# Kernel tuning notes

Measured on AMD Instinct MI355X. Metric: run time of the kernel, lower is better.

## Reference

```python
import jax, jax.numpy as jnp
import numpy as np


def setup_inputs() -> dict:
    key = jax.random.key(0)
    ks = jax.random.split(key, 8)
    N, T, U = 8, 200, 50
    E = D = J = 512
    V = 500
    s = lambda k, shape, fan_in: jax.random.normal(k, shape, jnp.float32) / np.sqrt(fan_in)
    return {
        "encoder_out": jax.random.normal(ks[0], (N, T, E), jnp.float32),
        "decoder_out": jax.random.normal(ks[1], (N, U, D), jnp.float32),
        "W_enc": s(ks[2], (J, E), E),
        "b_enc": jax.random.normal(ks[3], (J,), jnp.float32) * 0.01,
        "W_dec": s(ks[4], (J, D), D),
        "b_dec": jax.random.normal(ks[5], (J,), jnp.float32) * 0.01,
        "W_out": s(ks[6], (V, J), J),
        "b_out": jax.random.normal(ks[7], (V,), jnp.float32) * 0.01,
    }


def reference(encoder_out, decoder_out, W_enc, b_enc, W_dec, b_dec, W_out, b_out):
    # Project encoder (N,T,E)->(N,T,J) and decoder (N,U,D)->(N,U,J).
    enc_p = jnp.einsum("nte,je->ntj", encoder_out, W_enc) + b_enc
    dec_p = jnp.einsum("nud,jd->nuj", decoder_out, W_dec) + b_dec
    # Broadcast add -> (N,T,U,J), tanh, then linear to vocab -> (N,T,U,V).
    activations = jnp.tanh(enc_p[:, :, None, :] + dec_p[:, None, :, :])
    logits = jnp.einsum("ntuj,vj->ntuv", activations, W_out) + b_out
    return logits
```

## Files before the change

kernel.cpp:

```cpp
#include <hip/hip_runtime.h>
#include <hip/hip_bf16.h>
#include <stdint.h>

#define JD 512
#define VV 500

typedef short short8 __attribute__((ext_vector_type(8)));
typedef short short4v __attribute__((ext_vector_type(4)));
typedef float floatx4 __attribute__((ext_vector_type(4)));

__device__ inline short f2bf(float f) {
    uint32_t u = __float_as_uint(f);
    uint32_t r = (u + 0x7FFFu + ((u >> 16) & 1u)) >> 16;
    return (short)r;
}

__device__ inline float fast_tanh(float x) {
    float e = __builtin_amdgcn_exp2f(x * 2.8853900817779268f);
    return 1.0f - 2.0f * __builtin_amdgcn_rcpf(e + 1.0f);
}

__global__ __launch_bounds__(256) void prep_kernel(
    const float* __restrict__ Wout, short* __restrict__ WbF)
{
    int j = blockIdx.x * 256 + threadIdx.x;
    int l16  = j & 15;
    int q4   = (j >> 4) & 3;
    int ks   = (j >> 6) & 15;
    int vblk = j >> 10;
    int v  = vblk * 16 + l16;
    int k0 = ks * 32 + q4 * 8;
    short8 o;
    if (v < VV) {
        const float4* p = (const float4*)(Wout + (size_t)v * JD + k0);
        float4 a = p[0], b = p[1];
        o[0] = f2bf(a.x); o[1] = f2bf(a.y); o[2] = f2bf(a.z); o[3] = f2bf(a.w);
        o[4] = f2bf(b.x); o[5] = f2bf(b.y); o[6] = f2bf(b.z); o[7] = f2bf(b.w);
    } else {
        o = (short8){0,0,0,0,0,0,0,0};
    }
    *(short8*)(WbF + (size_t)j * 8) = o;
}

#define PST 72
__global__ __launch_bounds__(256) void proj_gemm(
    const float* __restrict__ enc, const float* __restrict__ dec,
    const float* __restrict__ Wenc, const float* __restrict__ Wdec,
    const float* __restrict__ b_enc, const float* __restrict__ b_dec,
    float* __restrict__ enc_p, float* __restrict__ dec_p)
{
    __shared__ short As[64 * PST];
    __shared__ short Bs[64 * PST];
    int bx = blockIdx.x, by = blockIdx.y;
    const float* A; const float* W; const float* bias; float* C; int M;
    if (bx < 25) { A = enc; W = Wenc; bias = b_enc; C = enc_p; M = 1600; }
    else { bx -= 25; A = dec; W = Wdec; bias = b_dec; C = dec_p; M = 400; }

    int tid = threadIdx.x;
    int lane = tid & 63, wv = tid >> 6;
    int wm = wv >> 1, wn = wv & 1;
    int l16 = lane & 15, q4 = lane >> 4;

    int ra = tid >> 2, ha = tid & 3;
    int m_st = bx * 64 + ra;
    bool valid = m_st < M;
    int wrow = by * 64 + ra;

    floatx4 acc[2][2];
    #pragma unroll
    for (int a = 0; a < 2; a++)
        #pragma unroll
        for (int b = 0; b < 2; b++) acc[a][b] = (floatx4){0.f, 0.f, 0.f, 0.f};

    for (int kk = 0; kk < 8; kk++) {
        int k0 = kk * 64;
        __syncthreads();
        {
            float4 v0 = make_float4(0.f, 0.f, 0.f, 0.f);
            float4 v1 = v0, v2 = v0, v3 = v0;
            if (valid) {
                const float4* p = (const float4*)(A + (size_t)m_st * JD + k0 + ha * 16);
                v0 = p[0]; v1 = p[1]; v2 = p[2]; v3 = p[3];
            }
            short8 o0, o1;
            o0[0] = f2bf(v0.x); o0[1] = f2bf(v0.y); o0[2] = f2bf(v0.z); o0[3] = f2bf(v0.w);
            o0[4] = f2bf(v1.x); o0[5] = f2bf(v1.y); o0[6] = f2bf(v1.z); o0[7] = f2bf(v1.w);
            o1[0] = f2bf(v2.x); o1[1] = f2bf(v2.y); o1[2] = f2bf(v2.z); o1[3] = f2bf(v2.w);
            o1[4] = f2bf(v3.x); o1[5] = f2bf(v3.y); o1[6] = f2bf(v3.z); o1[7] = f2bf(v3.w);
            *(short8*)&As[ra * PST + ha * 16]     = o0;
            *(short8*)&As[ra * PST + ha * 16 + 8] = o1;

            const float4* pb = (const float4*)(W + (size_t)wrow * JD + k0 + ha * 16);
            float4 w0 = pb[0], w1 = pb[1], w2 = pb[2], w3 = pb[3];
            short8 p0, p1;
            p0[0] = f2bf(w0.x); p0[1] = f2bf(w0.y); p0[2] = f2bf(w0.z); p0[3] = f2bf(w0.w);
            p0[4] = f2bf(w1.x); p0[5] = f2bf(w1.y); p0[6] = f2bf(w1.z); p0[7] = f2bf(w1.w);
            p1[0] = f2bf(w2.x); p1[1] = f2bf(w2.y); p1[2] = f2bf(w2.z); p1[3] = f2bf(w2.w);
            p1[4] = f2bf(w3.x); p1[5] = f2bf(w3.y); p1[6] = f2bf(w3.z); p1[7] = f2bf(w3.w);
            *(short8*)&Bs[ra * PST + ha * 16]     = p0;
            *(short8*)&Bs[ra * PST + ha * 16 + 8] = p1;
        }
        __syncthreads();
        #pragma unroll
        for (int h2 = 0; h2 < 2; h2++) {
            short8 af[2], bf[2];
            #pragma unroll
            for (int im = 0; im < 2; im++)
                af[im] = *(const short8*)&As[(wm * 32 + im * 16 + l16) * PST + h2 * 32 + q4 * 8];
            #pragma unroll
            for (int in = 0; in < 2; in++)
                bf[in] = *(const short8*)&Bs[(wn * 32 + in * 16 + l16) * PST + h2 * 32 + q4 * 8];
            #pragma unroll
            for (int im = 0; im < 2; im++)
                #pragma unroll
                for (int in = 0; in < 2; in++)
                    acc[im][in] = __builtin_amdgcn_mfma_f32_16x16x32_bf16(
                        af[im], bf[in], acc[im][in], 0, 0, 0);
        }
    }
    #pragma unroll
    for (int im = 0; im < 2; im++) {
        int mb = bx * 64 + wm * 32 + im * 16 + q4 * 4;
        #pragma unroll
        for (int rr = 0; rr < 4; rr++) {
            int m = mb + rr;
            if (m < M) {
                #pragma unroll
                for (int in = 0; in < 2; in++) {
                    int j = by * 64 + wn * 32 + in * 16 + l16;
                    C[(size_t)m * JD + j] = acc[im][in][rr] + bias[j];
                }
            }
        }
    }
}

#define AST 520
__global__ __launch_bounds__(256, 2) void fused_joiner(
    const float* __restrict__ enc_p, const float* __restrict__ dec_p,
    const short* __restrict__ WbF, const float* __restrict__ b_out,
    float* __restrict__ out)
{
    __shared__ short As[64 * AST];
    int tid = threadIdx.x;
    int bx = blockIdx.x;

    {
        int rsub = tid >> 7;
        int jf = (tid & 127) * 4;
        #pragma unroll 4
        for (int pass = 0; pass < 32; pass++) {
            int row = pass * 2 + rsub;
            int m = bx * 64 + row;
            int er = m / 50;
            int n  = m / 10000;
            int dr = n * 50 + (m - er * 50);
            float4 e = *(const float4*)(enc_p + (size_t)er * JD + jf);
            float4 d = *(const float4*)(dec_p + (size_t)dr * JD + jf);
            short4v o;
            o[0] = f2bf(fast_tanh(e.x + d.x));
            o[1] = f2bf(fast_tanh(e.y + d.y));
            o[2] = f2bf(fast_tanh(e.z + d.z));
            o[3] = f2bf(fast_tanh(e.w + d.w));
            *(short4v*)&As[row * AST + jf] = o;
        }
    }
    __syncthreads();

    int lane = tid & 63, wn = tid >> 6;
    int l16 = lane & 15, q4 = lane >> 4;

    floatx4 acc[4][8];
    #pragma unroll
    for (int a = 0; a < 4; a++)
        #pragma unroll
        for (int b = 0; b < 8; b++) acc[a][b] = (floatx4){0.f, 0.f, 0.f, 0.f};

    int abase[4];
    #pragma unroll
    for (int im = 0; im < 4; im++)
        abase[im] = (im * 16 + l16) * AST + q4 * 8;
    int boff[8];
    #pragma unroll
    for (int in = 0; in < 8; in++)
        boff[in] = (wn * 8 + in) * 8192 + q4 * 128 + l16 * 8;

    short8 b0[8], b1[8];
    #pragma unroll
    for (int in = 0; in < 8; in++)
        b0[in] = *(const short8*)(WbF + boff[in]);

    for (int ks = 0; ks < 16; ks += 2) {
        #pragma unroll
        for (int in = 0; in < 8; in++)
            b1[in] = *(const short8*)(WbF + boff[in] + (ks + 1) * 512);
        {
            int k0 = ks * 32;
            short8 af[4];
            #pragma unroll
            for (int im = 0; im < 4; im++)
                af[im] = *(const short8*)&As[abase[im] + k0];
            #pragma unroll
            for (int im = 0; im < 4; im++)
                #pragma unroll
                for (int in = 0; in < 8; in++)
                    acc[im][in] = __builtin_amdgcn_mfma_f32_16x16x32_bf16(
                        af[im], b0[in], acc[im][in], 0, 0, 0);
        }
        if (ks + 2 < 16) {
            #pragma unroll
            for (int in = 0; in < 8; in++)
                b0[in] = *(const short8*)(WbF + boff[in] + (ks + 2) * 512);
        }
        {
            int k1 = (ks + 1) * 32;
            short8 af[4];
            #pragma unroll
            for (int im = 0; im < 4; im++)
                af[im] = *(const short8*)&As[abase[im] + k1];
            #pragma unroll
            for (int im = 0; im < 4; im++)
                #pragma unroll
                for (int in = 0; in < 8; in++)
                    acc[im][in] = __builtin_amdgcn_mfma_f32_16x16x32_bf16(
                        af[im], b1[in], acc[im][in], 0, 0, 0);
        }
    }

    float bo[8];
    #pragma unroll
    for (int in = 0; in < 8; in++) {
        int v = wn * 128 + in * 16 + l16;
        bo[in] = (v < VV) ? b_out[v] : 0.f;
    }
    #pragma unroll
    for (int im = 0; im < 4; im++) {
        int mb = bx * 64 + im * 16 + q4 * 4;
        #pragma unroll
        for (int rr = 0; rr < 4; rr++) {
            size_t orow = (size_t)(mb + rr) * VV;
            #pragma unroll
            for (int in = 0; in < 8; in++) {
                int v = wn * 128 + in * 16 + l16;
                if (v < VV) out[orow + v] = acc[im][in][rr] + bo[in];
            }
        }
    }
}

extern "C" void kernel_launch(void* const* d_in, const int* in_sizes, int n_in,
                              void* d_out, int out_size, void* d_ws, size_t ws_size,
                              hipStream_t stream)
{
    const float* enc   = (const float*)d_in[0];
    const float* dec   = (const float*)d_in[1];
    const float* Wenc  = (const float*)d_in[2];
    const float* b_enc = (const float*)d_in[3];
    const float* Wdec  = (const float*)d_in[4];
    const float* b_dec = (const float*)d_in[5];
    const float* Wout  = (const float*)d_in[6];
    const float* b_out = (const float*)d_in[7];
    float* out = (float*)d_out;

    char* ws = (char*)d_ws;
    short* WbF   = (short*)(ws + 0);
    float* enc_p = (float*)(ws + 524288);
    float* dec_p = (float*)(ws + 3801088);

    prep_kernel<<<128, 256, 0, stream>>>(Wout, WbF);
    proj_gemm<<<dim3(32, 8), 256, 0, stream>>>(enc, dec, Wenc, Wdec,
                                               b_enc, b_dec, enc_p, dec_p);
    fused_joiner<<<1250, 256, 0, stream>>>(enc_p, dec_p, WbF, b_out, out);
}
```

Baseline: 250.5 us.

## Split joiner tile across 8 waves, re-layout packed W_out, use nontemporal stores

The fused joiner block grows from 4 to 8 waves, each computing a 32x128 sub-tile instead of 64x128, so accumulators halve and more waves can be resident per CU. The packed bf16 W_out layout is reordered so each k-step's fragments for a wave are contiguous. The software double-buffering of B fragments is dropped. Output logits are written with nontemporal stores to avoid polluting cache. The cost is that each B fragment is now loaded by two waves instead of one, and latency hiding relies on occupancy rather than explicit prefetch.

```diff
diff --git a/kernel.cpp b/kernel.cpp
--- a/kernel.cpp
+++ b/kernel.cpp
@@ -24,11 +24,12 @@
     const float* __restrict__ Wout, short* __restrict__ WbF)
 {
     int j = blockIdx.x * 256 + threadIdx.x;
-    int l16  = j & 15;
-    int q4   = (j >> 4) & 3;
-    int ks   = (j >> 6) & 15;
-    int vblk = j >> 10;
-    int v  = vblk * 16 + l16;
+    int l16 = j & 15;
+    int q4  = (j >> 4) & 3;
+    int in  = (j >> 6) & 7;
+    int wn  = (j >> 9) & 3;
+    int ks  = j >> 11;
+    int v  = wn * 128 + in * 16 + l16;
     int k0 = ks * 32 + q4 * 8;
     short8 o;
     if (v < VV) {
@@ -136,7 +137,7 @@
 }
 
 #define AST 520
-__global__ __launch_bounds__(256, 2) void fused_joiner(
+__global__ __launch_bounds__(512, 4) void fused_joiner(
     const float* __restrict__ enc_p, const float* __restrict__ dec_p,
     const short* __restrict__ WbF, const float* __restrict__ b_out,
     float* __restrict__ out)
@@ -149,8 +150,8 @@
         int rsub = tid >> 7;
         int jf = (tid & 127) * 4;
         #pragma unroll 4
-        for (int pass = 0; pass < 32; pass++) {
-            int row = pass * 2 + rsub;
+        for (int pass = 0; pass < 16; pass++) {
+            int row = pass * 4 + rsub;
             int m = bx * 64 + row;
             int er = m / 50;
             int n  = m / 10000;
@@ -167,64 +168,40 @@
     }
     __syncthreads();
 
-    int lane = tid & 63, wn = tid >> 6;
+    int lane = tid & 63, wv = tid >> 6;
+    int wm = wv >> 2, wn = wv & 3;
     int l16 = lane & 15, q4 = lane >> 4;
 
-    floatx4 acc[4][8];
-    #pragma unroll
-    for (int a = 0; a < 4; a++)
+    floatx4 acc[2][8];
+    #pragma unroll
+    for (int a = 0; a < 2; a++)
         #pragma unroll
         for (int b = 0; b < 8; b++) acc[a][b] = (floatx4){0.f, 0.f, 0.f, 0.f};
 
-    int abase[4];
-    #pragma unroll
-    for (int im = 0; im < 4; im++)
-        abase[im] = (im * 16 + l16) * AST + q4 * 8;
-    int boff[8];
-    #pragma unroll
-    for (int in = 0; in < 8; in++)
-        boff[in] = (wn * 8 + in) * 8192 + q4 * 128 + l16 * 8;
-
-    short8 b0[8], b1[8];
-    #pragma unroll
-    for (int in = 0; in < 8; in++)
-        b0[in] = *(const short8*)(WbF + boff[in]);
-
-    for (int ks = 0; ks < 16; ks += 2) {
+    int abase[2];
+    #pragma unroll
+    for (int im = 0; im < 2; im++)
+        abase[im] = (wm * 32 + im * 16 + l16) * AST + q4 * 8;
+
+    const short* wp = WbF + wn * 4096 + q4 * 128 + l16 * 8;
+
+    for (int ks = 0; ks < 16; ks++) {
+        short8 bfr[8];
         #pragma unroll
         for (int in = 0; in < 8; in++)
-            b1[in] = *(const short8*)(WbF + boff[in] + (ks + 1) * 512);
-        {
-            int k0 = ks * 32;
-            short8 af[4];
-            #pragma unroll
-            for (int im = 0; im < 4; im++)
-                af[im] = *(const short8*)&As[abase[im] + k0];
-            #pragma unroll
-            for (int im = 0; im < 4; im++)
-                #pragma unroll
-                for (int in = 0; in < 8; in++)
-                    acc[im][in] = __builtin_amdgcn_mfma_f32_16x16x32_bf16(
-                        af[im], b0[in], acc[im][in], 0, 0, 0);
-        }
-        if (ks + 2 < 16) {
+            bfr[in] = *(const short8*)(wp + in * 512);
+        short8 af[2];
+        int k0 = ks * 32;
+        #pragma unroll
+        for (int im = 0; im < 2; im++)
+            af[im] = *(const short8*)&As[abase[im] + k0];
+        #pragma unroll
+        for (int im = 0; im < 2; im++)
             #pragma unroll
             for (int in = 0; in < 8; in++)
-                b0[in] = *(const short8*)(WbF + boff[in] + (ks + 2) * 512);
-        }
-        {
-            int k1 = (ks + 1) * 32;
-            short8 af[4];
-            #pragma unroll
-            for (int im = 0; im < 4; im++)
-                af[im] = *(const short8*)&As[abase[im] + k1];
-            #pragma unroll
-            for (int im = 0; im < 4; im++)
-                #pragma unroll
-                for (int in = 0; in < 8; in++)
-                    acc[im][in] = __builtin_amdgcn_mfma_f32_16x16x32_bf16(
-                        af[im], b1[in], acc[im][in], 0, 0, 0);
-        }
+                acc[im][in] = __builtin_amdgcn_mfma_f32_16x16x32_bf16(
+                    af[im], bfr[in], acc[im][in], 0, 0, 0);
+        wp += 16384;
     }
 
     float bo[8];
@@ -234,15 +211,17 @@
         bo[in] = (v < VV) ? b_out[v] : 0.f;
     }
     #pragma unroll
-    for (int im = 0; im < 4; im++) {
-        int mb = bx * 64 + im * 16 + q4 * 4;
+    for (int im = 0; im < 2; im++) {
+        int mb = bx * 64 + wm * 32 + im * 16 + q4 * 4;
         #pragma unroll
         for (int rr = 0; rr < 4; rr++) {
             size_t orow = (size_t)(mb + rr) * VV;
             #pragma unroll
             for (int in = 0; in < 8; in++) {
                 int v = wn * 128 + in * 16 + l16;
-                if (v < VV) out[orow + v] = acc[im][in][rr] + bo[in];
+                if (v < VV)
+                    __builtin_nontemporal_store(acc[im][in][rr] + bo[in],
+                                                &out[orow + v]);
             }
         }
     }
@@ -270,5 +249,5 @@
     prep_kernel<<<128, 256, 0, stream>>>(Wout, WbF);
     proj_gemm<<<dim3(32, 8), 256, 0, stream>>>(enc, dec, Wenc, Wdec,
                                                b_enc, b_dec, enc_p, dec_p);
-    fused_joiner<<<1250, 256, 0, stream>>>(enc_p, dec_p, WbF, b_out, out);
-}
+    fused_joiner<<<1250, 512, 0, stream>>>(enc_p, dec_p, WbF, b_out, out);
+}
```

New measurement: 257.1 us. +2.6%, slower.
